# Kernel tuning notes

Measured on AMD Instinct MI355X. Metric: run time of the kernel, lower is better.

The kernel has to match this reference:

```python
import jax, jax.numpy as jnp
import numpy as np

NUM_LAYERS = 3  # from init_kwargs


def setup_inputs() -> dict:
    key = jax.random.key(0)
    k1, k2, k3 = jax.random.split(key, 3)
    n_users, n_items, d, E = 200000, 100000, 32, 5000000
    n = n_users + n_items
    return {
        "edge_index": jax.random.randint(k1, (2, E), 0, n, dtype=jnp.int64),
        "n_users": n_users,
        "n_items": n_items,
        "user_emb": 0.1 * jax.random.normal(k2, (n_users, d), dtype=jnp.float32),
        "item_emb": 0.1 * jax.random.normal(k3, (n_items, d), dtype=jnp.float32),
    }


def reference(edge_index, n_users, n_items, user_emb, item_emb):
    n = n_users + n_items
    x = jnp.concatenate([user_emb, item_emb], axis=0)  # [n, d]
    src, dst = edge_index[0], edge_index[1]

    # degree of each node as destination (matches torch scatter_add on dst)
    deg = jax.ops.segment_sum(jnp.ones(dst.shape[0], dtype=x.dtype), dst,
                              num_segments=n)  # [n]
    dprod = deg[src] * deg[dst]  # [E]
    # (deg_src*deg_dst)^-0.5, with inf (zero degree) replaced by 0
    norm = jnp.where(dprod > 0, dprod ** -0.5, jnp.zeros_like(dprod))

    acc = x  # running sum over layer embeddings (layer 0 included)
    for _ in range(NUM_LAYERS):
        msg = x[src] * norm[:, None]                          # gather + scale [E, d]
        x = jax.ops.segment_sum(msg, dst, num_segments=n)     # scatter-add  [n, d]
        acc = acc + x
    x = acc / jnp.asarray(NUM_LAYERS + 1, dtype=x.dtype)      # mean over layers
    return (x[:n_users], x[n_users:])
```

## Files before the change

### kernel.cpp

```cpp
#include <hip/hip_runtime.h>
#include <hip/hip_fp16.h>


#define D 32
#define TILE 8192
#define BNODES 128
#define MAXB2 2560
#define SPT 10
#define CAP 2560
#define NKEY 8192
#define KPT 32

__global__ void __launch_bounds__(256)
msplit_kernel(const int* __restrict__ src, const int* __restrict__ dst, int E, int nb,
              int* __restrict__ qcur, unsigned* __restrict__ estrm) {
    __shared__ unsigned buf[TILE];
    __shared__ int hist[MAXB2], exc_[MAXB2], gbase[MAXB2], off[MAXB2];
    __shared__ int wsum[256];
    int t = threadIdx.x;
    int tile0 = blockIdx.x * TILE;
    if (tile0 >= E) return;
    int cnt = min(TILE, E - tile0);

    for (int i = t; i < MAXB2; i += 256) hist[i] = 0;
    __syncthreads();
    for (int i = t; i < cnt; i += 256)
        atomicAdd(&hist[dst[tile0 + i] >> 7], 1);
    __syncthreads();

    int lsum = 0;
    #pragma unroll
    for (int s = 0; s < SPT; ++s) lsum += hist[t * SPT + s];
    wsum[t] = lsum;
    __syncthreads();
    for (int o = 1; o < 256; o <<= 1) {
        int a = (t >= o) ? wsum[t - o] : 0;
        __syncthreads();
        wsum[t] += a;
        __syncthreads();
    }
    int run = (t > 0) ? wsum[t - 1] : 0;
    #pragma unroll
    for (int s = 0; s < SPT; ++s) {
        int b = t * SPT + s;
        int h = hist[b];
        exc_[b] = run;
        off[b]  = run;
        run += h;
        gbase[b] = (h > 0) ? (b * CAP + atomicAdd(&qcur[b], h)) : 0;
    }
    __syncthreads();

    for (int i = t; i < cnt; i += 256) {
        int d = dst[tile0 + i];
        int s = src[tile0 + i];
        int b = d >> 7;
        int pos = atomicAdd(&off[b], 1);
        buf[pos] = ((unsigned)(d & (BNODES - 1)) << 19) | (unsigned)s;
    }
    __syncthreads();

    for (int i = t; i < cnt; i += 256) {
        int lo = 0, hi = nb - 1;
        while (lo < hi) { int mid = (lo + hi + 1) >> 1; if (exc_[mid] <= i) lo = mid; else hi = mid - 1; }
        estrm[gbase[lo] + (i - exc_[lo])] = buf[i];
    }
}

__global__ void __launch_bounds__(256)
binfill3_kernel(unsigned* estrm, const int* __restrict__ ecnt, int n,
                float* __restrict__ rd, float* __restrict__ ird,
                int* __restrict__ rstart, int* __restrict__ rlen, int* col) {
    int b = blockIdx.x;
    int lo = b << 7;
    int nn = min(BNODES, n - lo);
    int base = b * CAP;
    int ec = ecnt[b];
    __shared__ unsigned ebuf[CAP];
    __shared__ int kcnt[NKEY];
    __shared__ int dcnt[BNODES];
    __shared__ int wsum[256];
    int t = threadIdx.x;
    for (int i = t; i < NKEY; i += 256) kcnt[i] = 0;
    if (t < BNODES) dcnt[t] = 0;
    __syncthreads();
    for (int i = t; i < ec; i += 256) {
        unsigned pk = estrm[base + i];
        ebuf[i] = pk;
        int dlo = (int)(pk >> 19);
        int st  = (int)((pk & 0x7FFFF) >> 13);
        atomicAdd(&kcnt[(dlo << 6) | st], 1);
        atomicAdd(&dcnt[dlo], 1);
    }
    __syncthreads();
    int lsum = 0;
    #pragma unroll
    for (int s = 0; s < KPT; ++s) lsum += kcnt[t * KPT + s];
    wsum[t] = lsum;
    __syncthreads();
    for (int o = 1; o < 256; o <<= 1) {
        int a = (t >= o) ? wsum[t - o] : 0;
        __syncthreads();
        wsum[t] += a;
        __syncthreads();
    }
    int run = (t > 0) ? wsum[t - 1] : 0;
    #pragma unroll
    for (int s = 0; s < KPT; ++s) {
        int idx = t * KPT + s;
        int c = kcnt[idx];
        kcnt[idx] = run;
        run += c;
    }
    __syncthreads();
    if (t < nn) {
        int c = dcnt[t];
        rstart[lo + t] = base + kcnt[t << 6];
        rlen[lo + t]   = c;
        rd[lo + t]  = (c > 0) ? rsqrtf((float)c) : 0.0f;
        ird[lo + t] = (c > 0) ? sqrtf((float)c)  : 0.0f;
    }
    __syncthreads();
    for (int i = t; i < ec; i += 256) {
        unsigned pk = ebuf[i];
        int key = (int)((pk >> 19) << 6) | (int)((pk & 0x7FFFF) >> 13);
        int p = atomicAdd(&kcnt[key], 1);
        col[base + p] = (int)(pk & 0x7FFFF);
    }
}

__global__ void init_kernel(const float* __restrict__ ue, const float* __restrict__ ie,
                            const float* __restrict__ rd, int nu32, int tot32,
                            __half* __restrict__ y0) {
    int gid = blockIdx.x * blockDim.x + threadIdx.x;
    int i2 = gid * 2;
    if (i2 < tot32) {
        float v0 = (i2 < nu32) ? ue[i2] : ie[i2 - nu32];
        float v1 = (i2 < nu32) ? ue[i2 + 1] : ie[i2 + 1 - nu32];
        float r = rd[i2 >> 5];
        *reinterpret_cast<__half2*>(y0 + i2) = __floats2half2_rn(r * v0, r * v1);
    }
}

__global__ void __launch_bounds__(256)
layer_kernel(const int* __restrict__ rstart, const int* __restrict__ rlen,
             const int* __restrict__ col, const float* __restrict__ rd,
             const __half* __restrict__ yin, __half* __restrict__ yout, int n) {
    int gid = blockIdx.x * blockDim.x + threadIdx.x;
    int node = gid >> 3;
    int q = gid & 7;
    if (node >= n) return;
    int e0 = rstart[node];
    int e1 = e0 + rlen[node];
    float4 s = make_float4(0.f, 0.f, 0.f, 0.f);
    for (int base = e0; base < e1; base += 8) {
        int idx = base + q;
        int c = (idx < e1) ? col[idx] : 0;
        int m = min(8, e1 - base);
        for (int j = 0; j < m; ++j) {
            int cj = __shfl(c, j, 8);
            uint2 u = *reinterpret_cast<const uint2*>(yin + (size_t)cj * D + q * 4);
            float2 f0 = __half22float2(*reinterpret_cast<__half2*>(&u.x));
            float2 f1 = __half22float2(*reinterpret_cast<__half2*>(&u.y));
            s.x += f0.x; s.y += f0.y; s.z += f1.x; s.w += f1.y;
        }
    }
    float r = rd[node];
    float r2 = r * r;
    __half2 o0 = __floats2half2_rn(r2 * s.x, r2 * s.y);
    __half2 o1 = __floats2half2_rn(r2 * s.z, r2 * s.w);
    uint2 o;
    o.x = *reinterpret_cast<unsigned*>(&o0);
    o.y = *reinterpret_cast<unsigned*>(&o1);
    *reinterpret_cast<uint2*>(yout + (size_t)node * D + q * 4) = o;
}

__global__ void merge_kernel(const float* __restrict__ ue, const float* __restrict__ ie,
                             const float* __restrict__ ird,
                             const __half* __restrict__ y1, const __half* __restrict__ y2,
                             const __half* __restrict__ y3,
                             int nu32, int tot32, float* __restrict__ out) {
    int gid = blockIdx.x * blockDim.x + threadIdx.x;
    int i2 = gid * 2;
    if (i2 < tot32) {
        float v0 = (i2 < nu32) ? ue[i2] : ie[i2 - nu32];
        float v1 = (i2 < nu32) ? ue[i2 + 1] : ie[i2 + 1 - nu32];
        float iv = ird[i2 >> 5];
        float2 a = __half22float2(*reinterpret_cast<const __half2*>(y1 + i2));
        float2 b = __half22float2(*reinterpret_cast<const __half2*>(y2 + i2));
        float2 c = __half22float2(*reinterpret_cast<const __half2*>(y3 + i2));
        float o0 = 0.25f * (v0 + (a.x + b.x + c.x) * iv);
        float o1 = 0.25f * (v1 + (a.y + b.y + c.y) * iv);
        *reinterpret_cast<float2*>(out + i2) = make_float2(o0, o1);
    }
}

static inline char* alloc256(char*& p, size_t bytes) {
    uintptr_t q = ((uintptr_t)p + 255) & ~(uintptr_t)255;
    char* r = (char*)q;
    p = r + bytes;
    return r;
}

extern "C" void kernel_launch(void* const* d_in, const int* in_sizes, int n_in,
                              void* d_out, int out_size, void* d_ws, size_t ws_size,
                              hipStream_t stream) {
    const int*   edge = (const int*)d_in[0];
    const float* ue   = (const float*)d_in[3];
    const float* ie   = (const float*)d_in[4];
    int E  = in_sizes[0] / 2;
    int nu = in_sizes[3] / D;
    int ni = in_sizes[4] / D;
    int n  = nu + ni;
    int nb = (n + BNODES - 1) >> 7;
    const int* src = edge;
    const int* dst = edge + E;
    float* out = (float*)d_out;

    char* p = (char*)d_ws;
    int*      qcur   = (int*)alloc256(p, (size_t)(MAXB2 + 1) * 4);
    float*    rd     = (float*)alloc256(p, (size_t)n * 4);
    float*    ird    = (float*)alloc256(p, (size_t)n * 4);
    int*      rstart = (int*)alloc256(p, (size_t)n * 4);
    int*      rlen   = (int*)alloc256(p, (size_t)n * 4);
    unsigned* estrm  = (unsigned*)alloc256(p, (size_t)nb * CAP * 4);
    int*      col    = (int*)estrm;
    __half*   yA     = (__half*)alloc256(p, (size_t)n * D * 2);
    __half*   yB     = (__half*)alloc256(p, (size_t)n * D * 2);
    __half*   yC     = (__half*)alloc256(p, (size_t)n * D * 2);

    hipMemsetAsync(qcur, 0, (size_t)(MAXB2 + 1) * 4, stream);

    msplit_kernel<<<(E + TILE - 1) / TILE, 256, 0, stream>>>(src, dst, E, nb, qcur, estrm);
    binfill3_kernel<<<nb, 256, 0, stream>>>(estrm, qcur, n, rd, ird, rstart, rlen, col);

    int tot32 = n * D;
    init_kernel<<<(n * 16 + 255) / 256, 256, 0, stream>>>(ue, ie, rd, nu * D, tot32, yA);

    int tot8 = n * 8;
    layer_kernel<<<(tot8 + 255) / 256, 256, 0, stream>>>(rstart, rlen, col, rd, yA, yB, n);
    layer_kernel<<<(tot8 + 255) / 256, 256, 0, stream>>>(rstart, rlen, col, rd, yB, yC, n);
    layer_kernel<<<(tot8 + 255) / 256, 256, 0, stream>>>(rstart, rlen, col, rd, yC, yA, n);

    merge_kernel<<<(n * 16 + 255) / 256, 256, 0, stream>>>(ue, ie, ird, yB, yC, yA,
                                                           nu * D, tot32, out);
}
```

Baseline: 657.5 us.

## Use 1024-node destination bins for edge bucketing and CSR construction

Destination nodes are now grouped into 1024-node bins instead of 128-node bins, giving about 293 bins of 18432 capacity each. The partition kernel's scan covers 512 bins with two elements per thread, and the per-bin sort uses 32 source strata with a 32768-entry shared key histogram. Because a bin's edges no longer fit in shared memory, they are re-read from global memory and written to a separate col array. The aim is fewer, more contiguous scatter destinations in the split pass. The cost is heavier per-block shared-memory work, fewer blocks in the bin-fill pass, a coarser source sort for gather locality, and overflow risk if a bin exceeds its capacity.

```diff
diff --git a/kernel.cpp b/kernel.cpp
--- a/kernel.cpp
+++ b/kernel.cpp
@@ -4,98 +4,89 @@
 
 #define D 32
 #define TILE 8192
-#define BNODES 128
-#define MAXB2 2560
-#define SPT 10
-#define CAP 2560
-#define NKEY 8192
-#define KPT 32
+#define MAXB 512
+#define CAP 18432
+#define NST 32
+#define NKEY4 32768
+#define KPT4 128
 
 __global__ void __launch_bounds__(256)
 msplit_kernel(const int* __restrict__ src, const int* __restrict__ dst, int E, int nb,
               int* __restrict__ qcur, unsigned* __restrict__ estrm) {
     __shared__ unsigned buf[TILE];
-    __shared__ int hist[MAXB2], exc_[MAXB2], gbase[MAXB2], off[MAXB2];
-    __shared__ int wsum[256];
+    __shared__ int hist[MAXB], exc[MAXB], gbase[MAXB], off[MAXB], sc[MAXB];
     int t = threadIdx.x;
     int tile0 = blockIdx.x * TILE;
     if (tile0 >= E) return;
     int cnt = min(TILE, E - tile0);
 
-    for (int i = t; i < MAXB2; i += 256) hist[i] = 0;
+    for (int i = t; i < MAXB; i += 256) hist[i] = 0;
     __syncthreads();
     for (int i = t; i < cnt; i += 256)
-        atomicAdd(&hist[dst[tile0 + i] >> 7], 1);
-    __syncthreads();
-
-    int lsum = 0;
-    #pragma unroll
-    for (int s = 0; s < SPT; ++s) lsum += hist[t * SPT + s];
-    wsum[t] = lsum;
-    __syncthreads();
-    for (int o = 1; o < 256; o <<= 1) {
-        int a = (t >= o) ? wsum[t - o] : 0;
-        __syncthreads();
-        wsum[t] += a;
-        __syncthreads();
-    }
-    int run = (t > 0) ? wsum[t - 1] : 0;
-    #pragma unroll
-    for (int s = 0; s < SPT; ++s) {
-        int b = t * SPT + s;
-        int h = hist[b];
-        exc_[b] = run;
-        off[b]  = run;
-        run += h;
-        gbase[b] = (h > 0) ? (b * CAP + atomicAdd(&qcur[b], h)) : 0;
-    }
+        atomicAdd(&hist[dst[tile0 + i] >> 10], 1);
+    __syncthreads();
+
+    int h0 = hist[t], h1 = hist[t + 256];
+    sc[t] = h0; sc[t + 256] = h1;
+    __syncthreads();
+    for (int o = 1; o < MAXB; o <<= 1) {
+        int a0 = (t >= o) ? sc[t - o] : 0;
+        int a1 = (t + 256 >= o) ? sc[t + 256 - o] : 0;
+        __syncthreads();
+        sc[t] += a0; sc[t + 256] += a1;
+        __syncthreads();
+    }
+    exc[t] = sc[t] - h0;
+    exc[t + 256] = sc[t + 256] - h1;
+    gbase[t]       = (h0 > 0) ? (t * CAP + atomicAdd(&qcur[t], h0))               : 0;
+    gbase[t + 256] = (h1 > 0) ? ((t + 256) * CAP + atomicAdd(&qcur[t + 256], h1)) : 0;
+    off[t] = exc[t];
+    off[t + 256] = exc[t + 256];
     __syncthreads();
 
     for (int i = t; i < cnt; i += 256) {
         int d = dst[tile0 + i];
         int s = src[tile0 + i];
-        int b = d >> 7;
+        int b = d >> 10;
         int pos = atomicAdd(&off[b], 1);
-        buf[pos] = ((unsigned)(d & (BNODES - 1)) << 19) | (unsigned)s;
+        buf[pos] = ((unsigned)(d & 1023) << 19) | (unsigned)s;
     }
     __syncthreads();
 
     for (int i = t; i < cnt; i += 256) {
         int lo = 0, hi = nb - 1;
-        while (lo < hi) { int mid = (lo + hi + 1) >> 1; if (exc_[mid] <= i) lo = mid; else hi = mid - 1; }
-        estrm[gbase[lo] + (i - exc_[lo])] = buf[i];
+        while (lo < hi) { int mid = (lo + hi + 1) >> 1; if (exc[mid] <= i) lo = mid; else hi = mid - 1; }
+        estrm[gbase[lo] + (i - exc[lo])] = buf[i];
     }
 }
 
 __global__ void __launch_bounds__(256)
-binfill3_kernel(unsigned* estrm, const int* __restrict__ ecnt, int n,
-                float* __restrict__ rd, float* __restrict__ ird,
-                int* __restrict__ rstart, int* __restrict__ rlen, int* col) {
+binfill4_kernel(const unsigned* __restrict__ estrm, const int* __restrict__ ecnt,
+                int n, float* __restrict__ rd, float* __restrict__ ird,
+                int* __restrict__ rstart, int* __restrict__ rlen,
+                int* __restrict__ col) {
     int b = blockIdx.x;
-    int lo = b << 7;
-    int nn = min(BNODES, n - lo);
+    int lo = b << 10;
+    int nn = min(1024, n - lo);
     int base = b * CAP;
     int ec = ecnt[b];
-    __shared__ unsigned ebuf[CAP];
-    __shared__ int kcnt[NKEY];
-    __shared__ int dcnt[BNODES];
+    __shared__ int kcnt[NKEY4];
+    __shared__ int dcnt[1024];
     __shared__ int wsum[256];
     int t = threadIdx.x;
-    for (int i = t; i < NKEY; i += 256) kcnt[i] = 0;
-    if (t < BNODES) dcnt[t] = 0;
+    for (int i = t; i < NKEY4; i += 256) kcnt[i] = 0;
+    for (int i = t; i < 1024; i += 256) dcnt[i] = 0;
     __syncthreads();
     for (int i = t; i < ec; i += 256) {
         unsigned pk = estrm[base + i];
-        ebuf[i] = pk;
         int dlo = (int)(pk >> 19);
-        int st  = (int)((pk & 0x7FFFF) >> 13);
-        atomicAdd(&kcnt[(dlo << 6) | st], 1);
+        int st  = (int)((pk & 0x7FFFF) >> 14);
+        atomicAdd(&kcnt[(dlo << 5) | st], 1);
         atomicAdd(&dcnt[dlo], 1);
     }
     __syncthreads();
     int lsum = 0;
-    #pragma unroll
-    for (int s = 0; s < KPT; ++s) lsum += kcnt[t * KPT + s];
+    for (int s = 0; s < KPT4; ++s) lsum += kcnt[t * KPT4 + s];
     wsum[t] = lsum;
     __syncthreads();
     for (int o = 1; o < 256; o <<= 1) {
@@ -105,25 +96,24 @@
         __syncthreads();
     }
     int run = (t > 0) ? wsum[t - 1] : 0;
-    #pragma unroll
-    for (int s = 0; s < KPT; ++s) {
-        int idx = t * KPT + s;
+    for (int s = 0; s < KPT4; ++s) {
+        int idx = t * KPT4 + s;
         int c = kcnt[idx];
         kcnt[idx] = run;
         run += c;
     }
     __syncthreads();
-    if (t < nn) {
-        int c = dcnt[t];
-        rstart[lo + t] = base + kcnt[t << 6];
-        rlen[lo + t]   = c;
-        rd[lo + t]  = (c > 0) ? rsqrtf((float)c) : 0.0f;
-        ird[lo + t] = (c > 0) ? sqrtf((float)c)  : 0.0f;
+    for (int i = t; i < nn; i += 256) {
+        int c = dcnt[i];
+        rstart[lo + i] = base + kcnt[i << 5];
+        rlen[lo + i]   = c;
+        rd[lo + i]  = (c > 0) ? rsqrtf((float)c) : 0.0f;
+        ird[lo + i] = (c > 0) ? sqrtf((float)c)  : 0.0f;
     }
     __syncthreads();
     for (int i = t; i < ec; i += 256) {
-        unsigned pk = ebuf[i];
-        int key = (int)((pk >> 19) << 6) | (int)((pk & 0x7FFFF) >> 13);
+        unsigned pk = estrm[base + i];
+        int key = (int)((pk >> 19) << 5) | (int)((pk & 0x7FFFF) >> 14);
         int p = atomicAdd(&kcnt[key], 1);
         col[base + p] = (int)(pk & 0x7FFFF);
     }
@@ -212,27 +202,27 @@
     int nu = in_sizes[3] / D;
     int ni = in_sizes[4] / D;
     int n  = nu + ni;
-    int nb = (n + BNODES - 1) >> 7;
+    int nb = (n + 1023) >> 10;
     const int* src = edge;
     const int* dst = edge + E;
     float* out = (float*)d_out;
 
     char* p = (char*)d_ws;
-    int*      qcur   = (int*)alloc256(p, (size_t)(MAXB2 + 1) * 4);
+    int*      qcur   = (int*)alloc256(p, (size_t)(MAXB + 1) * 4);
     float*    rd     = (float*)alloc256(p, (size_t)n * 4);
     float*    ird    = (float*)alloc256(p, (size_t)n * 4);
     int*      rstart = (int*)alloc256(p, (size_t)n * 4);
     int*      rlen   = (int*)alloc256(p, (size_t)n * 4);
     unsigned* estrm  = (unsigned*)alloc256(p, (size_t)nb * CAP * 4);
-    int*      col    = (int*)estrm;
+    int*      col    = (int*)alloc256(p, (size_t)nb * CAP * 4);
     __half*   yA     = (__half*)alloc256(p, (size_t)n * D * 2);
     __half*   yB     = (__half*)alloc256(p, (size_t)n * D * 2);
     __half*   yC     = (__half*)alloc256(p, (size_t)n * D * 2);
 
-    hipMemsetAsync(qcur, 0, (size_t)(MAXB2 + 1) * 4, stream);
+    hipMemsetAsync(qcur, 0, (size_t)(MAXB + 1) * 4, stream);
 
     msplit_kernel<<<(E + TILE - 1) / TILE, 256, 0, stream>>>(src, dst, E, nb, qcur, estrm);
-    binfill3_kernel<<<nb, 256, 0, stream>>>(estrm, qcur, n, rd, ird, rstart, rlen, col);
+    binfill4_kernel<<<nb, 256, 0, stream>>>(estrm, qcur, n, rd, ird, rstart, rlen, col);
 
     int tot32 = n * D;
     init_kernel<<<(n * 16 + 255) / 256, 256, 0, stream>>>(ue, ie, rd, nu * D, tot32, yA);
```

Measured after the change: 571.4 us. 1.15x faster.
